# Kernel optimization log

Hardware: AMD Instinct MI355X
Metric: run time of the kernel (lower is better)

Reference implementation:

```python
import jax, jax.numpy as jnp
import numpy as np

H = 32       # num query heads
KVH = 8      # num kv heads
D = 2048     # hidden_dim
B = 2
S = 2048
HD = D // H  # head_dim = 64


def setup_inputs() -> dict:
    key = jax.random.key(0)
    ks = jax.random.split(key, 9)
    s = 1.0 / np.sqrt(D).astype(np.float32)
    kvd = KVH * HD
    x = jax.random.normal(ks[0], (B, S, D), jnp.float32)
    # weights stored as (in, out) so forward is x @ W + b
    Wq = jax.random.normal(ks[1], (D, D), jnp.float32) * s
    bq = jax.random.normal(ks[2], (D,), jnp.float32) * 0.01
    Wk = jax.random.normal(ks[3], (D, kvd), jnp.float32) * s
    bk = jax.random.normal(ks[4], (kvd,), jnp.float32) * 0.01
    Wv = jax.random.normal(ks[5], (D, kvd), jnp.float32) * s
    bv = jax.random.normal(ks[6], (kvd,), jnp.float32) * 0.01
    Wo = jax.random.normal(ks[7], (D, D), jnp.float32) * s
    bo = jax.random.normal(ks[8], (D,), jnp.float32) * 0.01
    return {"x": x, "Wq": Wq, "bq": bq, "Wk": Wk, "bk": bk,
            "Wv": Wv, "bv": bv, "Wo": Wo, "bo": bo}


def reference(x, Wq, bq, Wk, bk, Wv, bv, Wo, bo):
    b, s, d = x.shape
    hd = d // H
    # projections -> (B, heads, S, head_dim)
    Q = (x @ Wq + bq).reshape(b, s, H, hd).transpose(0, 2, 1, 3)
    K = (x @ Wk + bk).reshape(b, s, KVH, hd).transpose(0, 2, 1, 3)
    V = (x @ Wv + bv).reshape(b, s, KVH, hd).transpose(0, 2, 1, 3)
    # GQA: repeat KV heads to match query heads (repeat_interleave on head dim)
    rep = H // KVH
    Kr = jnp.repeat(K, rep, axis=1)
    Vr = jnp.repeat(V, rep, axis=1)
    scale = jnp.asarray(1.0 / np.sqrt(hd), x.dtype)
    scores = jnp.einsum('bhqd,bhkd->bhqk', Q, Kr) * scale
    attn = jax.nn.softmax(scores, axis=-1)
    out = jnp.einsum('bhqk,bhkd->bhqd', attn, Vr)
    out = out.transpose(0, 2, 1, 3).reshape(b, s, d)
    return out @ Wo + bo
```

## Files before the change

### kernel.cpp

```cpp
#include <hip/hip_runtime.h>
#include <hip/hip_bf16.h>
#include <cstdint>

#define NH 32
#define NKVH 8
#define DM 2048
#define NB 2
#define SQ 2048
#define HDIM 64
#define MT (NB*SQ)
#define KVD (NKVH*HDIM)

typedef __attribute__((ext_vector_type(8))) short short8;
typedef __attribute__((ext_vector_type(4))) short short4v;
typedef __attribute__((ext_vector_type(4))) float f32x4;
typedef __attribute__((ext_vector_type(16))) float f32x16;
typedef __attribute__((ext_vector_type(4))) unsigned int uint4v;

static __device__ __forceinline__ short f2b(float f) {
  uint32_t u = __builtin_bit_cast(uint32_t, f);
  u += 0x7FFFu + ((u >> 16) & 1u);
  return (short)(u >> 16);
}

static __device__ __forceinline__ uint32_t cvt_pk_bf16(float lo, float hi) {
  uint32_t r;
  asm("v_cvt_pk_bf16_f32 %0, %1, %2" : "=v"(r) : "v"(lo), "v"(hi));
  return r;
}

#define GLL16(g, l) __builtin_amdgcn_global_load_lds(                          \
    (__attribute__((address_space(1))) const void*)(g),                        \
    (__attribute__((address_space(3))) void*)(l), 16, 0, 0)

__global__ void cast_x_kernel(const float* __restrict__ x, short* __restrict__ xb, int n4) {
  int i = blockIdx.x * blockDim.x + threadIdx.x;
  const int stride = gridDim.x * blockDim.x;
  for (; i < n4; i += stride) {
    const float4 v = ((const float4*)x)[i];
    short4v o;
    o.x = f2b(v.x); o.y = f2b(v.y); o.z = f2b(v.z); o.w = f2b(v.w);
    ((short4v*)xb)[i] = o;
  }
}

__global__ void transpose_cast_kernel(const float* __restrict__ W, short* __restrict__ Wt,
                                      int Kd, int Nd) {
  __shared__ float tile[32][33];
  const int n0 = blockIdx.x * 32, k0 = blockIdx.y * 32;
  const int tx = threadIdx.x & 31, ty = threadIdx.x >> 5;
#pragma unroll
  for (int i = 0; i < 4; i++)
    tile[ty + i * 8][tx] = W[(size_t)(k0 + ty + i * 8) * Nd + n0 + tx];
  __syncthreads();
#pragma unroll
  for (int i = 0; i < 4; i++)
    Wt[(size_t)(n0 + ty + i * 8) * Kd + k0 + tx] = f2b(tile[tx][ty + i * 8]);
}

template <int EPI>
__global__ __launch_bounds__(256) void gemm_kernel(const short* __restrict__ A,
                                                   const short* __restrict__ Bt,
                                                   const float* __restrict__ bias,
                                                   void* __restrict__ Cout, int N) {
  __shared__ __align__(16) short As[2 * 128 * 32];
  __shared__ __align__(16) short Bs[2 * 128 * 32];
  const int K = DM;
  const int tid = threadIdx.x;
  const int wave = tid >> 6, lane = tid & 63;
  const int g = lane >> 4, r16 = lane & 15;
  const int m0 = blockIdx.y * 128, n0 = blockIdx.x * 128;
  const int wr = wave >> 1, wc = wave & 1;

  f32x4 acc[4][4];
#pragma unroll
  for (int i = 0; i < 4; i++)
#pragma unroll
    for (int j = 0; j < 4; j++) acc[i][j] = (f32x4){0.f, 0.f, 0.f, 0.f};

  const int srow = lane >> 2, sslot = lane & 3;
  const short* aS0 = A + (size_t)(m0 + (wave * 2 + 0) * 16 + srow) * K + sslot * 8;
  const short* aS1 = A + (size_t)(m0 + (wave * 2 + 1) * 16 + srow) * K + sslot * 8;
  const short* bS0 = Bt + (size_t)(n0 + (wave * 2 + 0) * 16 + srow) * K + sslot * 8;
  const short* bS1 = Bt + (size_t)(n0 + (wave * 2 + 1) * 16 + srow) * K + sslot * 8;
  short* aD0 = As + (wave * 2 + 0) * 512;
  short* aD1 = As + (wave * 2 + 1) * 512;
  short* bD0 = Bs + (wave * 2 + 0) * 512;
  short* bD1 = Bs + (wave * 2 + 1) * 512;

  GLL16(aS0, aD0);
  GLL16(aS1, aD1);
  GLL16(bS0, bD0);
  GLL16(bS1, bD1);
  __syncthreads();

  int buf = 0;
  for (int k0 = 0; k0 < K; k0 += 32) {
    if (k0 + 32 < K) {
      const int nb2 = (buf ^ 1) * 4096;
      GLL16(aS0 + k0 + 32, aD0 + nb2);
      GLL16(aS1 + k0 + 32, aD1 + nb2);
      GLL16(bS0 + k0 + 32, bD0 + nb2);
      GLL16(bS1 + k0 + 32, bD1 + nb2);
    }
    const short* Ac = As + buf * 4096;
    const short* Bc = Bs + buf * 4096;
    short8 af[4], bf[4];
#pragma unroll
    for (int mi = 0; mi < 4; mi++)
      af[mi] = *(const short8*)&Ac[(wr * 64 + mi * 16 + r16) * 32 + g * 8];
#pragma unroll
    for (int ni = 0; ni < 4; ni++)
      bf[ni] = *(const short8*)&Bc[(wc * 64 + ni * 16 + r16) * 32 + g * 8];
    __builtin_amdgcn_s_setprio(1);
#pragma unroll
    for (int mi = 0; mi < 4; mi++)
#pragma unroll
      for (int ni = 0; ni < 4; ni++)
        acc[mi][ni] = __builtin_amdgcn_mfma_f32_16x16x32_bf16(af[mi], bf[ni], acc[mi][ni], 0, 0, 0);
    __builtin_amdgcn_s_setprio(0);
    __syncthreads();
    buf ^= 1;
  }

  float bvv[4];
#pragma unroll
  for (int ni = 0; ni < 4; ni++) bvv[ni] = bias[n0 + wc * 64 + ni * 16 + r16];
#pragma unroll
  for (int mi = 0; mi < 4; mi++) {
#pragma unroll
    for (int ni = 0; ni < 4; ni++) {
      const int n = n0 + wc * 64 + ni * 16 + r16;
#pragma unroll
      for (int j = 0; j < 4; j++) {
        const int m = m0 + wr * 64 + mi * 16 + g * 4 + j;
        const float v = acc[mi][ni][j] + bvv[ni];
        if (EPI == 0) {
          ((short*)Cout)[(size_t)m * N + n] = f2b(v);
        } else {
          ((float*)Cout)[(size_t)m * N + n] = v;
        }
      }
    }
  }
}

__global__ __launch_bounds__(256) void gemm_qkv_kernel(const short* __restrict__ A,
                                                       const short* __restrict__ Bt,
                                                       const float* __restrict__ bq,
                                                       const float* __restrict__ bk,
                                                       const float* __restrict__ bv,
                                                       short* __restrict__ Qout,
                                                       short* __restrict__ Kout,
                                                       short* __restrict__ Vout) {
  __shared__ __align__(16) short As[2 * 128 * 32];
  __shared__ __align__(16) short Bs[2 * 128 * 32];
  const int K = DM;
  const int tid = threadIdx.x;
  const int wave = tid >> 6, lane = tid & 63;
  const int g = lane >> 4, r16 = lane & 15;
  const int m0 = blockIdx.y * 128, n0 = blockIdx.x * 128;
  const int wr = wave >> 1, wc = wave & 1;

  f32x4 acc[4][4];
#pragma unroll
  for (int i = 0; i < 4; i++)
#pragma unroll
    for (int j = 0; j < 4; j++) acc[i][j] = (f32x4){0.f, 0.f, 0.f, 0.f};

  const int srow = lane >> 2, sslot = lane & 3;
  const short* aS0 = A + (size_t)(m0 + (wave * 2 + 0) * 16 + srow) * K + sslot * 8;
  const short* aS1 = A + (size_t)(m0 + (wave * 2 + 1) * 16 + srow) * K + sslot * 8;
  const short* bS0 = Bt + (size_t)(n0 + (wave * 2 + 0) * 16 + srow) * K + sslot * 8;
  const short* bS1 = Bt + (size_t)(n0 + (wave * 2 + 1) * 16 + srow) * K + sslot * 8;
  short* aD0 = As + (wave * 2 + 0) * 512;
  short* aD1 = As + (wave * 2 + 1) * 512;
  short* bD0 = Bs + (wave * 2 + 0) * 512;
  short* bD1 = Bs + (wave * 2 + 1) * 512;

  GLL16(aS0, aD0);
  GLL16(aS1, aD1);
  GLL16(bS0, bD0);
  GLL16(bS1, bD1);
  __syncthreads();

  int buf = 0;
  for (int k0 = 0; k0 < K; k0 += 32) {
    if (k0 + 32 < K) {
      const int nb2 = (buf ^ 1) * 4096;
      GLL16(aS0 + k0 + 32, aD0 + nb2);
      GLL16(aS1 + k0 + 32, aD1 + nb2);
      GLL16(bS0 + k0 + 32, bD0 + nb2);
      GLL16(bS1 + k0 + 32, bD1 + nb2);
    }
    const short* Ac = As + buf * 4096;
    const short* Bc = Bs + buf * 4096;
    short8 af[4], bf[4];
#pragma unroll
    for (int mi = 0; mi < 4; mi++)
      af[mi] = *(const short8*)&Ac[(wr * 64 + mi * 16 + r16) * 32 + g * 8];
#pragma unroll
    for (int ni = 0; ni < 4; ni++)
      bf[ni] = *(const short8*)&Bc[(wc * 64 + ni * 16 + r16) * 32 + g * 8];
    __builtin_amdgcn_s_setprio(1);
#pragma unroll
    for (int mi = 0; mi < 4; mi++)
#pragma unroll
      for (int ni = 0; ni < 4; ni++)
        acc[mi][ni] = __builtin_amdgcn_mfma_f32_16x16x32_bf16(af[mi], bf[ni], acc[mi][ni], 0, 0, 0);
    __builtin_amdgcn_s_setprio(0);
    __syncthreads();
    buf ^= 1;
  }

  const int seg = (n0 < 2048) ? 0 : (n0 < 2560 ? 1 : 2);
  float bvv[4];
#pragma unroll
  for (int ni = 0; ni < 4; ni++) {
    const int n = n0 + wc * 64 + ni * 16 + r16;
    bvv[ni] = (seg == 0) ? bq[n] : (seg == 1 ? bk[n - 2048] : bv[n - 2560]);
  }
#pragma unroll
  for (int mi = 0; mi < 4; mi++) {
#pragma unroll
    for (int ni = 0; ni < 4; ni++) {
      const int n = n0 + wc * 64 + ni * 16 + r16;
#pragma unroll
      for (int j = 0; j < 4; j++) {
        const int m = m0 + wr * 64 + mi * 16 + g * 4 + j;
        const float v = acc[mi][ni][j] + bvv[ni];
        if (seg == 0) {
          Qout[(size_t)m * DM + n] = f2b(v);
        } else if (seg == 1) {
          Kout[(size_t)m * KVD + (n - 2048)] = f2b(v);
        } else {
          const int np = n - 2560;
          const int bb = m >> 11, s = m & (SQ - 1);
          const int kvh = np >> 6, d = np & 63;
          Vout[((size_t)((bb * NKVH + kvh) * HDIM + d) << 11) + s] = f2b(v);
        }
      }
    }
  }
}

__global__ __launch_bounds__(256, 2) void attn_kernel(const short* __restrict__ Qb,
                                                      const short* __restrict__ Kb,
                                                      const short* __restrict__ Vtb,
                                                      short* __restrict__ Ab) {
  __shared__ __align__(16) short Ks[2][64 * 64];
  __shared__ __align__(16) short Vs[2][64 * 64];
  __shared__ float alds[4][32];

  const int tid = threadIdx.x, wave = tid >> 6, lane = tid & 63;
  const int la31 = lane & 31, hi = lane >> 5;

  const int pb = blockIdx.x;
  const int lb = (pb & 7) * 128 + (pb >> 3);
  const int qb = lb & 15, h = (lb >> 4) & 31, b = lb >> 9;
  const int kvh = h >> 2;

  const float SCL = 0.18033688f;

  short8 qf[4];
  {
    const int qrow = b * SQ + qb * 128 + wave * 32 + la31;
    const short* qp = Qb + (size_t)qrow * DM + h * HDIM;
#pragma unroll
    for (int ks = 0; ks < 4; ks++)
      qf[ks] = *(const short8*)(qp + ks * 16 + hi * 8);
  }

  f32x16 zro;
#pragma unroll
  for (int r = 0; r < 16; r++) zro[r] = 0.f;

  f32x16 o[2];
#pragma unroll
  for (int nt = 0; nt < 2; nt++) o[nt] = zro;
  float l = 0.f;

  const int r3 = lane >> 3, sp = lane & 7;
  const int cs = (sp ^ r3) * 8;
  const int krow0 = wave * 16 + r3, krow1 = wave * 16 + 8 + r3;
  const short* kS0 = Kb + (size_t)(b * SQ + krow0) * KVD + kvh * HDIM + cs;
  const short* kS1 = Kb + (size_t)(b * SQ + krow1) * KVD + kvh * HDIM + cs;
  const short* vS0 = Vtb + (size_t)((b * NKVH + kvh) * HDIM + krow0) * SQ + cs;
  const short* vS1 = Vtb + (size_t)((b * NKVH + kvh) * HDIM + krow1) * SQ + cs;
  char* kD0base = (char*)&Ks[0][0] + (wave * 2 + 0) * 1024;
  char* kD1base = (char*)&Ks[0][0] + (wave * 2 + 1) * 1024;
  char* vD0base = (char*)&Vs[0][0] + (wave * 2 + 0) * 1024;
  char* vD1base = (char*)&Vs[0][0] + (wave * 2 + 1) * 1024;

  const int xr = (la31 & 7) << 4;

  GLL16(kS0, kD0base);
  GLL16(kS1, kD1base);
  GLL16(vS0, vD0base);
  GLL16(vS1, vD1base);
  __syncthreads();

  int cur = 0;
  for (int t = 0; t < SQ / 64; t++) {
    if (t + 1 < SQ / 64) {
      const int nxt = cur ^ 1;
      const size_t ko = (size_t)(t + 1) * 64 * KVD;
      const int vo = (t + 1) * 64;
      GLL16(kS0 + ko, kD0base + nxt * 8192);
      GLL16(kS1 + ko, kD1base + nxt * 8192);
      GLL16(vS0 + vo, vD0base + nxt * 8192);
      GLL16(vS1 + vo, vD1base + nxt * 8192);
    }

    f32x16 st[2];
#pragma unroll
    for (int tt = 0; tt < 2; tt++) {
      __builtin_amdgcn_s_setprio(1);
      {
        const short8 kf = *(const short8*)((const char*)&Ks[cur][0] +
            (32 * tt + la31) * 128 + ((16 * hi) ^ xr));
        st[tt] = __builtin_amdgcn_mfma_f32_32x32x16_bf16(kf, qf[0], zro, 0, 0, 0);
      }
#pragma unroll
      for (int ks = 1; ks < 4; ks++) {
        const short8 kf = *(const short8*)((const char*)&Ks[cur][0] +
            (32 * tt + la31) * 128 + ((32 * ks + 16 * hi) ^ xr));
        st[tt] = __builtin_amdgcn_mfma_f32_32x32x16_bf16(kf, qf[ks], st[tt], 0, 0, 0);
      }
      __builtin_amdgcn_s_setprio(0);
    }

#pragma unroll
    for (int tt = 0; tt < 2; tt++)
#pragma unroll
      for (int r = 0; r < 16; r++)
        st[tt][r] = exp2f(st[tt][r] * SCL);

    {
      float u[16];
#pragma unroll
      for (int i = 0; i < 16; i++) u[i] = st[0][i] + st[1][i];
#pragma unroll
      for (int off = 8; off >= 1; off >>= 1)
#pragma unroll
        for (int i = 0; i < off; i++) u[i] += u[i + off];
      float ps = u[0];
      ps += __shfl_xor(ps, 32);
      l += ps;
    }

    uint32_t pk[16];
#pragma unroll
    for (int tt = 0; tt < 2; tt++)
#pragma unroll
      for (int i = 0; i < 8; i++)
        pk[tt * 8 + i] = cvt_pk_bf16(st[tt][2 * i], st[tt][2 * i + 1]);

    short8 pa[4];
#pragma unroll
    for (int ks4 = 0; ks4 < 4; ks4++) {
      uint32_t w02[2], w13[2];
#pragma unroll
      for (int pp = 0; pp < 2; pp++) {
        const uint32_t a = pk[ks4 * 4 + pp];
        const uint32_t c = pk[ks4 * 4 + 2 + pp];
        const uint32_t u = hi ? a : c;
        const uint32_t s2 = (uint32_t)__shfl_xor((int)u, 32);
        w02[pp] = hi ? s2 : a;
        w13[pp] = hi ? c : s2;
      }
      uint4v wv;
      wv.x = w02[0]; wv.y = w02[1]; wv.z = w13[0]; wv.w = w13[1];
      pa[ks4] = __builtin_bit_cast(short8, wv);
    }

    __builtin_amdgcn_s_setprio(1);
#pragma unroll
    for (int nt = 0; nt < 2; nt++)
#pragma unroll
      for (int ks = 0; ks < 4; ks++) {
        const short8 vf = *(const short8*)((const char*)&Vs[cur][0] +
            (32 * nt + la31) * 128 + ((32 * ks + 16 * hi) ^ xr));
        o[nt] = __builtin_amdgcn_mfma_f32_32x32x16_bf16(pa[ks], vf, o[nt], 0, 0, 0);
      }
    __builtin_amdgcn_s_setprio(0);

    __syncthreads();
    cur ^= 1;
  }

  alds[wave][la31] = l;
  asm volatile("s_waitcnt lgkmcnt(0)" ::: "memory");
  float inv[16];
#pragma unroll
  for (int rr = 0; rr < 4; rr++) {
    const f32x4 lv = *(const f32x4*)&alds[wave][rr * 8 + hi * 4];
#pragma unroll
    for (int j = 0; j < 4; j++) inv[rr * 4 + j] = 1.0f / lv[j];
  }
  const int orow = b * SQ + qb * 128 + wave * 32;
#pragma unroll
  for (int nt = 0; nt < 2; nt++)
#pragma unroll
    for (int r = 0; r < 16; r++) {
      const int q = (r & 3) + 8 * (r >> 2) + 4 * hi;
      Ab[(size_t)(orow + q) * DM + h * HDIM + nt * 32 + la31] =
          f2b(o[nt][r] * inv[(r >> 2) * 4 + (r & 3)]);
    }
}

extern "C" void kernel_launch(void* const* d_in, const int* in_sizes, int n_in,
                              void* d_out, int out_size, void* d_ws, size_t ws_size,
                              hipStream_t stream) {
  const float* x  = (const float*)d_in[0];
  const float* Wq = (const float*)d_in[1];
  const float* bq = (const float*)d_in[2];
  const float* Wk = (const float*)d_in[3];
  const float* bk = (const float*)d_in[4];
  const float* Wv = (const float*)d_in[5];
  const float* bv = (const float*)d_in[6];
  const float* Wo = (const float*)d_in[7];
  const float* bo = (const float*)d_in[8];

  short* ws = (short*)d_ws;
  size_t off = 0;
  short* xb  = ws + off; off += (size_t)MT * DM;
  short* Wqt = ws + off; off += (size_t)DM * DM;
  short* Wkt = ws + off; off += (size_t)KVD * DM;
  short* Wvt = ws + off; off += (size_t)KVD * DM;
  short* Wot = ws + off; off += (size_t)DM * DM;
  short* Qb  = ws + off; off += (size_t)MT * DM;
  short* Kb  = ws + off; off += (size_t)MT * KVD;
  short* Vtb = ws + off; off += (size_t)MT * KVD;
  short* Ab  = ws + off;

  cast_x_kernel<<<2048, 256, 0, stream>>>(x, xb, MT * DM / 4);
  transpose_cast_kernel<<<dim3(DM / 32, DM / 32), 256, 0, stream>>>(Wq, Wqt, DM, DM);
  transpose_cast_kernel<<<dim3(KVD / 32, DM / 32), 256, 0, stream>>>(Wk, Wkt, DM, KVD);
  transpose_cast_kernel<<<dim3(KVD / 32, DM / 32), 256, 0, stream>>>(Wv, Wvt, DM, KVD);
  transpose_cast_kernel<<<dim3(DM / 32, DM / 32), 256, 0, stream>>>(Wo, Wot, DM, DM);

  gemm_qkv_kernel<<<dim3(3072 / 128, MT / 128), 256, 0, stream>>>(
      xb, Wqt, bq, bk, bv, Qb, Kb, Vtb);

  attn_kernel<<<NB * NH * (SQ / 128), 256, 0, stream>>>(Qb, Kb, Vtb, Ab);

  gemm_kernel<2><<<dim3(DM / 128, MT / 128), 256, 0, stream>>>(Ab, Wot, bo, d_out, DM);
}
```

Before: 362.3 us.

## Use a 5-stage LDS ring with vmcnt waits and XOR swizzle in GEMMs

Replaces the double-buffered GEMM main loop with a 5-slot shared-memory ring that keeps four K-tiles of global-to-LDS loads in flight. It waits with explicit vmcnt counts and one barrier per iteration instead of a full sync after compute. It also XOR-swizzles the 16-byte column slot in LDS to cut bank conflicts, and adds a min-blocks-per-CU hint of 2. This deepens latency hiding for the projection GEMMs at the cost of 80KB of LDS per block, which may limit occupancy. The hand-counted waits also depend on the load builtin being tracked by vmcnt.

Measured after the change: 390.0 us. 7.6% more time.

```diff
diff --git a/kernel.cpp b/kernel.cpp
--- a/kernel.cpp
+++ b/kernel.cpp
@@ -58,70 +58,73 @@
     Wt[(size_t)(n0 + ty + i * 8) * Kd + k0 + tx] = f2b(tile[tx][ty + i * 8]);
 }
 
+
+#define GEMM_RING_BODY(Kdim)                                                   \
+  const int tid = threadIdx.x;                                                 \
+  const int wave = tid >> 6, lane = tid & 63;                                  \
+  const int g = lane >> 4, r16 = lane & 15;                                    \
+  const int gx8 = (g ^ ((r16 >> 1) & 3)) * 8;           \
+  const int m0 = blockIdx.y * 128, n0 = blockIdx.x * 128;                      \
+  const int wr = wave >> 1, wc = wave & 1;                                     \
+  f32x4 acc[4][4];                                                             \
+  _Pragma("unroll") for (int i = 0; i < 4; i++)                                \
+    _Pragma("unroll") for (int j = 0; j < 4; j++)                              \
+      acc[i][j] = (f32x4){0.f, 0.f, 0.f, 0.f};                                 \
+  const int srow = lane >> 2, sslot = lane & 3;                                \
+  const int ssw8 = (sslot ^ ((srow >> 1) & 3)) * 8;  \
+  const short* aS0 = A + (size_t)(m0 + wave * 32 + srow) * Kdim + ssw8;        \
+  const short* aS1 = A + (size_t)(m0 + wave * 32 + 16 + srow) * Kdim + ssw8;   \
+  const short* bS0 = Bt + (size_t)(n0 + wave * 32 + srow) * Kdim + ssw8;       \
+  const short* bS1 = Bt + (size_t)(n0 + wave * 32 + 16 + srow) * Kdim + ssw8;  \
+  const int woff = wave * 1024;                                                \
+  const int nt = Kdim / 32;                                                    \
+  _Pragma("unroll") for (int p = 0; p < 4; p++) {    \
+    GLL16(aS0 + p * 32, As + p * 4096 + woff);                                 \
+    GLL16(aS1 + p * 32, As + p * 4096 + woff + 512);                           \
+    GLL16(bS0 + p * 32, Bs + p * 4096 + woff);                                 \
+    GLL16(bS1 + p * 32, Bs + p * 4096 + woff + 512);                           \
+  }                                                                            \
+  int rb = 0, wb = 4;                                                          \
+  for (int t = 0; t < nt; ++t) {                                               \
+    const int ahead = nt - 1 - t;                                              \
+    if (ahead >= 3)      asm volatile("s_waitcnt vmcnt(12)" ::: "memory");     \
+    else if (ahead == 2) asm volatile("s_waitcnt vmcnt(8)" ::: "memory");      \
+    else if (ahead == 1) asm volatile("s_waitcnt vmcnt(4)" ::: "memory");      \
+    else                 asm volatile("s_waitcnt vmcnt(0)" ::: "memory");      \
+    __builtin_amdgcn_s_barrier();                                              \
+    __builtin_amdgcn_sched_barrier(0);                                         \
+    if (t + 4 < nt) {                                                          \
+      const int k4 = (t + 4) * 32;                                             \
+      GLL16(aS0 + k4, As + wb * 4096 + woff);                                  \
+      GLL16(aS1 + k4, As + wb * 4096 + woff + 512);                            \
+      GLL16(bS0 + k4, Bs + wb * 4096 + woff);                                  \
+      GLL16(bS1 + k4, Bs + wb * 4096 + woff + 512);                            \
+      if (++wb == 5) wb = 0;                                                   \
+    }                                                                          \
+    const short* Ac = As + rb * 4096;                                          \
+    const short* Bc = Bs + rb * 4096;                                          \
+    if (++rb == 5) rb = 0;                                                     \
+    short8 af[4], bf[4];                                                       \
+    _Pragma("unroll") for (int mi = 0; mi < 4; mi++)                           \
+      af[mi] = *(const short8*)&Ac[(wr * 64 + mi * 16 + r16) * 32 + gx8];      \
+    _Pragma("unroll") for (int ni = 0; ni < 4; ni++)                           \
+      bf[ni] = *(const short8*)&Bc[(wc * 64 + ni * 16 + r16) * 32 + gx8];      \
+    __builtin_amdgcn_s_setprio(1);                                             \
+    _Pragma("unroll") for (int mi = 0; mi < 4; mi++)                           \
+      _Pragma("unroll") for (int ni = 0; ni < 4; ni++)                         \
+        acc[mi][ni] = __builtin_amdgcn_mfma_f32_16x16x32_bf16(                 \
+            af[mi], bf[ni], acc[mi][ni], 0, 0, 0);                             \
+    __builtin_amdgcn_s_setprio(0);                                             \
+  }
+
 template <int EPI>
-__global__ __launch_bounds__(256) void gemm_kernel(const short* __restrict__ A,
-                                                   const short* __restrict__ Bt,
-                                                   const float* __restrict__ bias,
-                                                   void* __restrict__ Cout, int N) {
-  __shared__ __align__(16) short As[2 * 128 * 32];
-  __shared__ __align__(16) short Bs[2 * 128 * 32];
-  const int K = DM;
-  const int tid = threadIdx.x;
-  const int wave = tid >> 6, lane = tid & 63;
-  const int g = lane >> 4, r16 = lane & 15;
-  const int m0 = blockIdx.y * 128, n0 = blockIdx.x * 128;
-  const int wr = wave >> 1, wc = wave & 1;
-
-  f32x4 acc[4][4];
-#pragma unroll
-  for (int i = 0; i < 4; i++)
-#pragma unroll
-    for (int j = 0; j < 4; j++) acc[i][j] = (f32x4){0.f, 0.f, 0.f, 0.f};
-
-  const int srow = lane >> 2, sslot = lane & 3;
-  const short* aS0 = A + (size_t)(m0 + (wave * 2 + 0) * 16 + srow) * K + sslot * 8;
-  const short* aS1 = A + (size_t)(m0 + (wave * 2 + 1) * 16 + srow) * K + sslot * 8;
-  const short* bS0 = Bt + (size_t)(n0 + (wave * 2 + 0) * 16 + srow) * K + sslot * 8;
-  const short* bS1 = Bt + (size_t)(n0 + (wave * 2 + 1) * 16 + srow) * K + sslot * 8;
-  short* aD0 = As + (wave * 2 + 0) * 512;
-  short* aD1 = As + (wave * 2 + 1) * 512;
-  short* bD0 = Bs + (wave * 2 + 0) * 512;
-  short* bD1 = Bs + (wave * 2 + 1) * 512;
-
-  GLL16(aS0, aD0);
-  GLL16(aS1, aD1);
-  GLL16(bS0, bD0);
-  GLL16(bS1, bD1);
-  __syncthreads();
-
-  int buf = 0;
-  for (int k0 = 0; k0 < K; k0 += 32) {
-    if (k0 + 32 < K) {
-      const int nb2 = (buf ^ 1) * 4096;
-      GLL16(aS0 + k0 + 32, aD0 + nb2);
-      GLL16(aS1 + k0 + 32, aD1 + nb2);
-      GLL16(bS0 + k0 + 32, bD0 + nb2);
-      GLL16(bS1 + k0 + 32, bD1 + nb2);
-    }
-    const short* Ac = As + buf * 4096;
-    const short* Bc = Bs + buf * 4096;
-    short8 af[4], bf[4];
-#pragma unroll
-    for (int mi = 0; mi < 4; mi++)
-      af[mi] = *(const short8*)&Ac[(wr * 64 + mi * 16 + r16) * 32 + g * 8];
-#pragma unroll
-    for (int ni = 0; ni < 4; ni++)
-      bf[ni] = *(const short8*)&Bc[(wc * 64 + ni * 16 + r16) * 32 + g * 8];
-    __builtin_amdgcn_s_setprio(1);
-#pragma unroll
-    for (int mi = 0; mi < 4; mi++)
-#pragma unroll
-      for (int ni = 0; ni < 4; ni++)
-        acc[mi][ni] = __builtin_amdgcn_mfma_f32_16x16x32_bf16(af[mi], bf[ni], acc[mi][ni], 0, 0, 0);
-    __builtin_amdgcn_s_setprio(0);
-    __syncthreads();
-    buf ^= 1;
-  }
+__global__ __launch_bounds__(256, 2) void gemm_kernel(const short* __restrict__ A,
+                                                      const short* __restrict__ Bt,
+                                                      const float* __restrict__ bias,
+                                                      void* __restrict__ Cout, int N) {
+  __shared__ __align__(16) short As[5 * 128 * 32];
+  __shared__ __align__(16) short Bs[5 * 128 * 32];
+  GEMM_RING_BODY(DM)
 
   float bvv[4];
 #pragma unroll
@@ -145,73 +148,17 @@
   }
 }
 
-__global__ __launch_bounds__(256) void gemm_qkv_kernel(const short* __restrict__ A,
-                                                       const short* __restrict__ Bt,
-                                                       const float* __restrict__ bq,
-                                                       const float* __restrict__ bk,
-                                                       const float* __restrict__ bv,
-                                                       short* __restrict__ Qout,
-                                                       short* __restrict__ Kout,
-                                                       short* __restrict__ Vout) {
-  __shared__ __align__(16) short As[2 * 128 * 32];
-  __shared__ __align__(16) short Bs[2 * 128 * 32];
-  const int K = DM;
-  const int tid = threadIdx.x;
-  const int wave = tid >> 6, lane = tid & 63;
-  const int g = lane >> 4, r16 = lane & 15;
-  const int m0 = blockIdx.y * 128, n0 = blockIdx.x * 128;
-  const int wr = wave >> 1, wc = wave & 1;
-
-  f32x4 acc[4][4];
-#pragma unroll
-  for (int i = 0; i < 4; i++)
-#pragma unroll
-    for (int j = 0; j < 4; j++) acc[i][j] = (f32x4){0.f, 0.f, 0.f, 0.f};
-
-  const int srow = lane >> 2, sslot = lane & 3;
-  const short* aS0 = A + (size_t)(m0 + (wave * 2 + 0) * 16 + srow) * K + sslot * 8;
-  const short* aS1 = A + (size_t)(m0 + (wave * 2 + 1) * 16 + srow) * K + sslot * 8;
-  const short* bS0 = Bt + (size_t)(n0 + (wave * 2 + 0) * 16 + srow) * K + sslot * 8;
-  const short* bS1 = Bt + (size_t)(n0 + (wave * 2 + 1) * 16 + srow) * K + sslot * 8;
-  short* aD0 = As + (wave * 2 + 0) * 512;
-  short* aD1 = As + (wave * 2 + 1) * 512;
-  short* bD0 = Bs + (wave * 2 + 0) * 512;
-  short* bD1 = Bs + (wave * 2 + 1) * 512;
-
-  GLL16(aS0, aD0);
-  GLL16(aS1, aD1);
-  GLL16(bS0, bD0);
-  GLL16(bS1, bD1);
-  __syncthreads();
-
-  int buf = 0;
-  for (int k0 = 0; k0 < K; k0 += 32) {
-    if (k0 + 32 < K) {
-      const int nb2 = (buf ^ 1) * 4096;
-      GLL16(aS0 + k0 + 32, aD0 + nb2);
-      GLL16(aS1 + k0 + 32, aD1 + nb2);
-      GLL16(bS0 + k0 + 32, bD0 + nb2);
-      GLL16(bS1 + k0 + 32, bD1 + nb2);
-    }
-    const short* Ac = As + buf * 4096;
-    const short* Bc = Bs + buf * 4096;
-    short8 af[4], bf[4];
-#pragma unroll
-    for (int mi = 0; mi < 4; mi++)
-      af[mi] = *(const short8*)&Ac[(wr * 64 + mi * 16 + r16) * 32 + g * 8];
-#pragma unroll
-    for (int ni = 0; ni < 4; ni++)
-      bf[ni] = *(const short8*)&Bc[(wc * 64 + ni * 16 + r16) * 32 + g * 8];
-    __builtin_amdgcn_s_setprio(1);
-#pragma unroll
-    for (int mi = 0; mi < 4; mi++)
-#pragma unroll
-      for (int ni = 0; ni < 4; ni++)
-        acc[mi][ni] = __builtin_amdgcn_mfma_f32_16x16x32_bf16(af[mi], bf[ni], acc[mi][ni], 0, 0, 0);
-    __builtin_amdgcn_s_setprio(0);
-    __syncthreads();
-    buf ^= 1;
-  }
+__global__ __launch_bounds__(256, 2) void gemm_qkv_kernel(const short* __restrict__ A,
+                                                          const short* __restrict__ Bt,
+                                                          const float* __restrict__ bq,
+                                                          const float* __restrict__ bk,
+                                                          const float* __restrict__ bv,
+                                                          short* __restrict__ Qout,
+                                                          short* __restrict__ Kout,
+                                                          short* __restrict__ Vout) {
+  __shared__ __align__(16) short As[5 * 128 * 32];
+  __shared__ __align__(16) short Bs[5 * 128 * 32];
+  GEMM_RING_BODY(DM)
 
   const int seg = (n0 < 2048) ? 0 : (n0 < 2560 ? 1 : 2);
   float bvv[4];
```
